# Performance work log

Measured on AMD Instinct MI355X. Metric: run time of the kernel, lower is better.

## Reference

```python
import jax, jax.numpy as jnp
import numpy as np

N = 4096
IN_DIM = 512
OUT_DIM = 64   # == d_head
HEADS = 8

def setup_inputs() -> dict:
    key = jax.random.key(0)
    ks = jax.random.split(key, 6)
    hd = OUT_DIM * HEADS  # 512
    s = 1.0 / np.sqrt(IN_DIM)
    x  = jax.random.normal(ks[0], (N, IN_DIM), dtype=jnp.float32)
    Wq = jax.random.uniform(ks[1], (hd, IN_DIM), minval=-s, maxval=s, dtype=jnp.float32)
    Wk = jax.random.uniform(ks[2], (hd, IN_DIM), minval=-s, maxval=s, dtype=jnp.float32)
    Wv = jax.random.uniform(ks[3], (hd, IN_DIM), minval=-s, maxval=s, dtype=jnp.float32)
    so = 1.0 / np.sqrt(hd)
    Wo = jax.random.uniform(ks[4], (OUT_DIM, hd), minval=-so, maxval=so, dtype=jnp.float32)
    bo = jax.random.uniform(ks[5], (OUT_DIM,), minval=-so, maxval=so, dtype=jnp.float32)
    return {"x": x, "Wq": Wq, "Wk": Wk, "Wv": Wv, "Wo": Wo, "bo": bo}

def reference(x, Wq, Wk, Wv, Wo, bo):
    n = x.shape[0]
    d_head = OUT_DIM
    Q = (x @ Wq.T).reshape(n, HEADS, d_head)
    K = (x @ Wk.T).reshape(n, HEADS, d_head)
    V = (x @ Wv.T).reshape(n, HEADS, d_head)
    # full softmax attention over all N nodes, per head
    attn = jnp.einsum('nhd,mhd->nhm', Q, K) / jnp.sqrt(jnp.float32(d_head))
    attn = jax.nn.softmax(attn, axis=-1)  # dropout p=0.0 -> identity
    out = jnp.einsum('nhm,mhd->nhd', attn, V)
    return out.reshape(n, HEADS * d_head) @ Wo.T + bo
```

## Files before the change

### kernel.cpp

```cpp
#include <hip/hip_runtime.h>

typedef unsigned short u16;
typedef unsigned int u32;
typedef __attribute__((ext_vector_type(8))) short bf16x8;
typedef __attribute__((ext_vector_type(4))) float f32x4;
typedef __attribute__((ext_vector_type(16))) float f32x16;
typedef __attribute__((ext_vector_type(4))) unsigned short u16x4;
typedef __attribute__((ext_vector_type(4))) unsigned int u32x4;

#define NSPLIT 8

__device__ __forceinline__ u16 f2b(float f) {
  u32 u = __builtin_bit_cast(u32, f);
  u32 r = (u + 0x7FFFu + ((u >> 16) & 1u)) >> 16;
  return (u16)r;
}

__device__ __forceinline__ f32x4 mfma16(bf16x8 a, bf16x8 b, f32x4 c) {
  return __builtin_amdgcn_mfma_f32_16x16x32_bf16(a, b, c, 0, 0, 0);
}
__device__ __forceinline__ f32x16 mfma32(bf16x8 a, bf16x8 b, f32x16 c) {
  return __builtin_amdgcn_mfma_f32_32x32x16_bf16(a, b, c, 0, 0, 0);
}
__device__ __forceinline__ u32 cvtpk(float lo, float hi) {
  u32 r;
  asm("v_cvt_pk_bf16_f32 %0, %1, %2" : "=v"(r) : "v"(lo), "v"(hi));
  return r;
}
__device__ __forceinline__ void pl32swap(u32& a, u32& b) {
  asm("v_permlane32_swap_b32 %0, %1" : "+v"(a), "+v"(b));
}

__global__ __launch_bounds__(256) void prep_kernel(
    const float* __restrict__ x, const float* __restrict__ wq,
    const float* __restrict__ wk, const float* __restrict__ Wo,
    const float* __restrict__ Wv,
    u16* __restrict__ xf, u16* __restrict__ wqf, u16* __restrict__ wkf,
    u16* __restrict__ wvof) {
  if (blockIdx.x < 1280) {
    int i = blockIdx.x * 256 + threadIdx.x;
    const float* src; u16* dst; int off; float scale = 1.0f;
    if (i < 262144)      { src = x;  dst = xf;  off = i; }
    else if (i < 294912) { src = wq; dst = wqf; off = i - 262144; scale = 0.18033688011112042f; }
    else                 { src = wk; dst = wkf; off = i - 294912; }
    int row = off >> 6;
    int c = (off & 63) * 8;
    int blk = row >> 4, lr = row & 15, kk = c >> 5, lg = (c >> 3) & 3;
    size_t fidx = ((((size_t)blk * 16 + kk) * 4 + lg) * 16 + lr) * 8;
    const float4* s4 = (const float4*)src;
    float4 a = s4[off * 2], b = s4[off * 2 + 1];
    u16x4 r0, r1;
    r0.x = f2b(a.x * scale); r0.y = f2b(a.y * scale);
    r0.z = f2b(a.z * scale); r0.w = f2b(a.w * scale);
    r1.x = f2b(b.x * scale); r1.y = f2b(b.y * scale);
    r1.z = f2b(b.z * scale); r1.w = f2b(b.w * scale);
    *(u16x4*)(dst + fidx) = r0;
    *(u16x4*)(dst + fidx + 4) = r1;
  } else {
    int t = (blockIdx.x - 1280) * 256 + threadIdx.x;
    int h = t >> 15, i = (t >> 9) & 63, j = t & 511;
    const float* worow = Wo + (size_t)i * 512 + h * 64;
    const float* wvcol = Wv + (size_t)(h * 64) * 512 + j;
    float s = 0.0f;
#pragma unroll 8
    for (int d = 0; d < 64; ++d) s += worow[d] * wvcol[(size_t)d * 512];
    int row = h * 64 + i;
    int cb = row >> 4, lr = row & 15, kk = j >> 5, lg = (j >> 3) & 3, jj = j & 7;
    wvof[((((size_t)cb * 16 + kk) * 4 + lg) * 16 + lr) * 8 + jj] = f2b(s);
  }
}

__global__ __launch_bounds__(256) void qkv_kernel(
    const u16* __restrict__ xf, const u16* __restrict__ wqf,
    const u16* __restrict__ wkf, const u16* __restrict__ wvof,
    u16* __restrict__ Qf, u16* __restrict__ Kf, u16* __restrict__ Vf) {
  int wave = threadIdx.x >> 6, lane = threadIdx.x & 63;
  int lr = lane & 15, lg = lane >> 4;
  int mode = blockIdx.y >> 2, cg = blockIdx.y & 3;
  const u16* W = (mode == 0) ? wqf : (mode == 1) ? wkf : wvof;
  f32x4 acc[2][8] = {};
  const u16* aB0 = xf + (size_t)(blockIdx.x * 8 + wave * 2) * 8192 + lg * 128 + lr * 8;
  const u16* bB0 = W + (size_t)(cg * 8) * 8192 + lg * 128 + lr * 8;
#pragma unroll 2
  for (int kk = 0; kk < 16; ++kk) {
    bf16x8 aF0 = *(const bf16x8*)(aB0 + kk * 512);
    bf16x8 aF1 = *(const bf16x8*)(aB0 + 8192 + kk * 512);
#pragma unroll
    for (int ni = 0; ni < 8; ++ni) {
      bf16x8 bF = *(const bf16x8*)(bB0 + (size_t)ni * 8192 + kk * 512);
      acc[0][ni] = mfma16(aF0, bF, acc[0][ni]);
      acc[1][ni] = mfma16(aF1, bF, acc[1][ni]);
    }
  }
  u16* dstBase = (mode == 0) ? Qf : (mode == 1) ? Kf : Vf;
#pragma unroll
  for (int rbi = 0; rbi < 2; ++rbi)
#pragma unroll
    for (int ni = 0; ni < 8; ++ni)
#pragma unroll
      for (int r = 0; r < 4; ++r) {
        int row = blockIdx.x * 128 + wave * 32 + rbi * 16 + lg * 4 + r;
        int colm = cg * 128 + ni * 16 + lr;
        int h = colm >> 6, d = colm & 63;
        u16 v = f2b(acc[rbi][ni][r]);
        u16* dst = dstBase + (size_t)h * 262144;
        if (mode < 2) {
          int kb = row >> 5, l31 = row & 31, s = (d >> 4) & 3, hi2 = (d >> 3) & 1, j = d & 7;
          dst[(((size_t)(kb * 4 + s) * 2 + hi2) * 32 + l31) * 8 + j] = v;
        } else {
          int kt = row >> 6, ks = (row >> 4) & 3, hi2 = (row >> 3) & 1, j = row & 7;
          dst[(((size_t)(kt * 4 + ks) * 2 + hi2) * 64 + d) * 8 + j] = v;
        }
      }
}

__global__ __launch_bounds__(256) void attn_kernel(
    const u16* __restrict__ Qf, const u16* __restrict__ Kf,
    const u16* __restrict__ Vf, float* __restrict__ Pacc,
    float* __restrict__ Pl) {
  int bid = blockIdx.x;
  int h = bid & 7, idx = bid >> 3;
  int c = idx & 7, qb = idx >> 3;
  int warp = threadIdx.x >> 6, lane = threadIdx.x & 63;
  int l31 = lane & 31, hi = lane >> 5;
  int q = qb * 128 + warp * 32 + l31;
  const u16* Qh = Qf + (size_t)h * 262144;
  const u16* Kh = Kf + (size_t)h * 262144;
  const u16* Vh = Vf + (size_t)h * 262144;

  int qb32 = qb * 4 + warp;
  bf16x8 qf[4];
#pragma unroll
  for (int s = 0; s < 4; ++s)
    qf[s] = *(const bf16x8*)(Qh + ((size_t)(qb32 * 4 + s) * 2 + hi) * 256 + l31 * 8);

  bf16x8 ka[4], kb[4];
  {
    int kb0 = (c * 512) >> 5;
#pragma unroll
    for (int s = 0; s < 4; ++s) {
      ka[s] = *(const bf16x8*)(Kh + ((size_t)(kb0 * 4 + s) * 2 + hi) * 256 + l31 * 8);
      kb[s] = *(const bf16x8*)(Kh + ((size_t)((kb0 + 1) * 4 + s) * 2 + hi) * 256 + l31 * 8);
    }
  }

  f32x16 o0 = {}, o1 = {};
  float l = 0.0f;

  for (int mt = 0; mt < 8; ++mt) {
    int kbase = c * 512 + mt * 64;
    int kt = kbase >> 6;
    f32x16 s0 = {}, s1 = {};
#pragma unroll
    for (int s = 0; s < 4; ++s) {
      s0 = mfma32(ka[s], qf[s], s0);
      s1 = mfma32(kb[s], qf[s], s1);
    }
    bf16x8 na[4], nb[4];
    if (mt < 7) {
      int nb0 = (kbase + 64) >> 5;
#pragma unroll
      for (int s = 0; s < 4; ++s) {
        na[s] = *(const bf16x8*)(Kh + ((size_t)(nb0 * 4 + s) * 2 + hi) * 256 + l31 * 8);
        nb[s] = *(const bf16x8*)(Kh + ((size_t)((nb0 + 1) * 4 + s) * 2 + hi) * 256 + l31 * 8);
      }
    }
    bf16x8 vf0[4], vf1[4];
#pragma unroll
    for (int ks = 0; ks < 4; ++ks) {
      const u16* vB = Vh + ((size_t)(kt * 4 + ks) * 2 + hi) * 512;
      vf0[ks] = *(const bf16x8*)(vB + l31 * 8);
      vf1[ks] = *(const bf16x8*)(vB + 256 + l31 * 8);
    }
#pragma unroll
    for (int r = 0; r < 16; ++r) s0[r] = __builtin_amdgcn_exp2f(s0[r]);
#pragma unroll
    for (int r = 0; r < 16; ++r) s1[r] = __builtin_amdgcn_exp2f(s1[r]);
    float u8[8];
#pragma unroll
    for (int i = 0; i < 8; ++i)
      u8[i] = (s0[i] + s0[i + 8]) + (s1[i] + s1[i + 8]);
    l += ((u8[0] + u8[1]) + (u8[2] + u8[3])) + ((u8[4] + u8[5]) + (u8[6] + u8[7]));
    u32 w[16];
#pragma unroll
    for (int i = 0; i < 8; ++i) {
      w[i]     = cvtpk(s0[2 * i], s0[2 * i + 1]);
      w[8 + i] = cvtpk(s1[2 * i], s1[2 * i + 1]);
    }
#pragma unroll
    for (int ks = 0; ks < 4; ++ks) {
      u32 a0 = w[4 * ks], b0 = w[4 * ks + 2];
      u32 a1 = w[4 * ks + 1], b1 = w[4 * ks + 3];
      pl32swap(a0, b0);
      pl32swap(a1, b1);
      u32x4 pw = {a0, a1, b0, b1};
      bf16x8 pb = __builtin_bit_cast(bf16x8, pw);
      o0 = mfma32(vf0[ks], pb, o0);
      o1 = mfma32(vf1[ks], pb, o1);
    }
#pragma unroll
    for (int s = 0; s < 4; ++s) { ka[s] = na[s]; kb[s] = nb[s]; }
  }
  l += __shfl_xor(l, 32);
  float* base = Pacc + ((size_t)(c * 8 + h) * 4096 + q) * 64;
#pragma unroll
  for (int g = 0; g < 4; ++g) {
    f32x4 v0 = {o0[4*g], o0[4*g+1], o0[4*g+2], o0[4*g+3]};
    f32x4 v1 = {o1[4*g], o1[4*g+1], o1[4*g+2], o1[4*g+3]};
    *(f32x4*)(base + 8 * g + 4 * hi) = v0;
    *(f32x4*)(base + 32 + 8 * g + 4 * hi) = v1;
  }
  if (!hi) Pl[(size_t)(c * 8 + h) * 4096 + q] = l;
}

__global__ __launch_bounds__(256) void combine_kernel(
    const float* __restrict__ Pacc, const float* __restrict__ Pl,
    const float* __restrict__ bo, float* __restrict__ out) {
  int t = blockIdx.x * 256 + threadIdx.x;
  int n = t >> 4, dp = (t & 15) * 4;
  f32x4 acc = {0, 0, 0, 0};
#pragma unroll
  for (int h = 0; h < 8; ++h) {
    float lt = 0.0f;
#pragma unroll
    for (int cc = 0; cc < NSPLIT; ++cc)
      lt += Pl[(size_t)(cc * 8 + h) * 4096 + n];
    float inv = 1.0f / lt;
    f32x4 oh = {0, 0, 0, 0};
#pragma unroll
    for (int cc = 0; cc < NSPLIT; ++cc) {
      f32x4 a = *(const f32x4*)(Pacc + (size_t)(cc * 8 + h) * 262144 + (size_t)n * 64 + dp);
      oh.x += a.x; oh.y += a.y; oh.z += a.z; oh.w += a.w;
    }
    acc.x += oh.x * inv; acc.y += oh.y * inv;
    acc.z += oh.z * inv; acc.w += oh.w * inv;
  }
  f32x4 b4 = *(const f32x4*)(bo + dp);
  acc.x += b4.x; acc.y += b4.y; acc.z += b4.z; acc.w += b4.w;
  *(f32x4*)(out + (size_t)n * 64 + dp) = acc;
}

extern "C" void kernel_launch(void* const* d_in, const int* in_sizes, int n_in,
                              void* d_out, int out_size, void* d_ws, size_t ws_size,
                              hipStream_t stream) {
  const float* x  = (const float*)d_in[0];
  const float* Wq = (const float*)d_in[1];
  const float* Wk = (const float*)d_in[2];
  const float* Wv = (const float*)d_in[3];
  const float* Wo = (const float*)d_in[4];
  const float* bo = (const float*)d_in[5];
  float* out = (float*)d_out;

  u16* xf   = (u16*)d_ws;
  u16* wqf  = xf + 2097152;
  u16* wkf  = wqf + 262144;
  u16* wvof = wkf + 262144;
  u16* Qf   = wvof + 262144;
  u16* Kf   = Qf + 2097152;
  u16* Vf   = Kf + 2097152;
  float* Pacc = (float*)(Vf + 2097152);
  float* Pl   = Pacc + (size_t)NSPLIT * 8 * 4096 * 64;
  (void)in_sizes; (void)n_in; (void)out_size; (void)ws_size;

  prep_kernel<<<2304, 256, 0, stream>>>(x, Wq, Wk, Wo, Wv, xf, wqf, wkf, wvof);
  qkv_kernel<<<dim3(32, 12), 256, 0, stream>>>(xf, wqf, wkf, wvof, Qf, Kf, Vf);
  attn_kernel<<<2048, 256, 0, stream>>>(Qf, Kf, Vf, Pacc, Pl);
  combine_kernel<<<256, 256, 0, stream>>>(Pacc, Pl, bo, out);
}
```

Before: 146.1 us.

## Stage QKV epilogue through LDS for vector stores; halve attention key splits

The QKV kernel now writes its accumulators into a swizzled shared-memory tile and then emits 16-byte vectorized global stores in the fragment layouts, replacing scattered 2-byte stores. The attention kernel drops from 8 to 4 key splits, so each block handles 1024 keys and the grid halves. The key loop is also restructured into a double-buffered helper that avoids register copies. Fewer splits shrink the partial-output traffic the combine kernel must read, at the cost of less parallelism and longer per-block serial work.

Result: faster. 137.4 us (-5.9%).

```diff
diff --git a/kernel.cpp b/kernel.cpp
--- a/kernel.cpp
+++ b/kernel.cpp
@@ -8,7 +8,7 @@
 typedef __attribute__((ext_vector_type(4))) unsigned short u16x4;
 typedef __attribute__((ext_vector_type(4))) unsigned int u32x4;
 
-#define NSPLIT 8
+#define NSPLIT 4
 
 __device__ __forceinline__ u16 f2b(float f) {
   u32 u = __builtin_bit_cast(u32, f);
@@ -70,10 +70,15 @@
   }
 }
 
+__device__ __forceinline__ int swz(int row, int colu16) {
+  return row * 256 + (((colu16) * 2) ^ ((row & 15) << 4));
+}
+
 __global__ __launch_bounds__(256) void qkv_kernel(
     const u16* __restrict__ xf, const u16* __restrict__ wqf,
     const u16* __restrict__ wkf, const u16* __restrict__ wvof,
     u16* __restrict__ Qf, u16* __restrict__ Kf, u16* __restrict__ Vf) {
+  __shared__ __align__(16) char tile[128 * 256];
   int wave = threadIdx.x >> 6, lane = threadIdx.x & 63;
   int lr = lane & 15, lg = lane >> 4;
   int mode = blockIdx.y >> 2, cg = blockIdx.y & 3;
@@ -92,26 +97,112 @@
       acc[1][ni] = mfma16(aF1, bF, acc[1][ni]);
     }
   }
+#pragma unroll
+  for (int rbi = 0; rbi < 2; ++rbi)
+#pragma unroll
+    for (int ni = 0; ni < 8; ++ni)
+#pragma unroll
+      for (int r = 0; r < 4; ++r) {
+        int row = wave * 32 + rbi * 16 + lg * 4 + r;
+        int col = ni * 16 + lr;
+        *(u16*)(tile + swz(row, col)) = f2b(acc[rbi][ni][r]);
+      }
+  __syncthreads();
   u16* dstBase = (mode == 0) ? Qf : (mode == 1) ? Kf : Vf;
-#pragma unroll
-  for (int rbi = 0; rbi < 2; ++rbi)
-#pragma unroll
-    for (int ni = 0; ni < 8; ++ni)
-#pragma unroll
-      for (int r = 0; r < 4; ++r) {
-        int row = blockIdx.x * 128 + wave * 32 + rbi * 16 + lg * 4 + r;
-        int colm = cg * 128 + ni * 16 + lr;
-        int h = colm >> 6, d = colm & 63;
-        u16 v = f2b(acc[rbi][ni][r]);
-        u16* dst = dstBase + (size_t)h * 262144;
-        if (mode < 2) {
-          int kb = row >> 5, l31 = row & 31, s = (d >> 4) & 3, hi2 = (d >> 3) & 1, j = d & 7;
-          dst[(((size_t)(kb * 4 + s) * 2 + hi2) * 32 + l31) * 8 + j] = v;
-        } else {
-          int kt = row >> 6, ks = (row >> 4) & 3, hi2 = (row >> 3) & 1, j = row & 7;
-          dst[(((size_t)(kt * 4 + ks) * 2 + hi2) * 64 + d) * 8 + j] = v;
-        }
+  if (mode < 2) {
+#pragma unroll
+    for (int it = 0; it < 8; ++it) {
+      int gid = wave * 8 + it;
+      int hh = gid >> 4, kbl = (gid >> 2) & 3, s = gid & 3;
+      int hi2 = lane >> 5, l31 = lane & 31;
+      int lrow = kbl * 32 + l31;
+      int col = hh * 64 + s * 16 + hi2 * 8;
+      u32x4 v = *(const u32x4*)(tile + swz(lrow, col));
+      int h = cg * 2 + hh, kb = blockIdx.x * 4 + kbl;
+      u16* dst = dstBase + (size_t)h * 262144 +
+                 (((size_t)(kb * 4 + s) * 2 + hi2) * 32 + l31) * 8;
+      *(u32x4*)dst = v;
+    }
+  } else {
+#pragma unroll
+    for (int it = 0; it < 8; ++it) {
+      int gid = wave * 8 + it;
+      int hh = gid >> 4, ktl = (gid >> 3) & 1, ks = (gid >> 1) & 3, hi2v = gid & 1;
+      int d = lane;
+      int r0 = ktl * 64 + ks * 16 + hi2v * 8;
+      int col = hh * 64 + d;
+      u32 wd[4];
+#pragma unroll
+      for (int jp = 0; jp < 4; ++jp) {
+        u32 lo = *(const u16*)(tile + swz(r0 + 2 * jp, col));
+        u32 hi = *(const u16*)(tile + swz(r0 + 2 * jp + 1, col));
+        wd[jp] = lo | (hi << 16);
       }
+      int h = cg * 2 + hh, kt = blockIdx.x * 2 + ktl;
+      u16* dst = dstBase + (size_t)h * 262144 +
+                 (((size_t)(kt * 4 + ks) * 2 + hi2v) * 64 + d) * 8;
+      u32x4 v = {wd[0], wd[1], wd[2], wd[3]};
+      *(u32x4*)dst = v;
+    }
+  }
+}
+
+struct KBuf { bf16x8 a[4], b[4]; };
+
+template <bool DOPREF>
+__device__ __forceinline__ void attn_step(
+    const u16* __restrict__ Kh, const u16* __restrict__ Vh,
+    const bf16x8 (&qf)[4], KBuf& cur, KBuf& nxt,
+    int kbase, int hi, int l31,
+    f32x16& o0, f32x16& o1, float& l) {
+  int kt = kbase >> 6;
+  f32x16 s0 = {}, s1 = {};
+#pragma unroll
+  for (int s = 0; s < 4; ++s) {
+    s0 = mfma32(cur.a[s], qf[s], s0);
+    s1 = mfma32(cur.b[s], qf[s], s1);
+  }
+  if (DOPREF) {
+    int nb0 = (kbase + 64) >> 5;
+#pragma unroll
+    for (int s = 0; s < 4; ++s) {
+      nxt.a[s] = *(const bf16x8*)(Kh + ((size_t)(nb0 * 4 + s) * 2 + hi) * 256 + l31 * 8);
+      nxt.b[s] = *(const bf16x8*)(Kh + ((size_t)((nb0 + 1) * 4 + s) * 2 + hi) * 256 + l31 * 8);
+    }
+  }
+  bf16x8 vf0[4], vf1[4];
+#pragma unroll
+  for (int ks = 0; ks < 4; ++ks) {
+    const u16* vB = Vh + ((size_t)(kt * 4 + ks) * 2 + hi) * 512;
+    vf0[ks] = *(const bf16x8*)(vB + l31 * 8);
+    vf1[ks] = *(const bf16x8*)(vB + 256 + l31 * 8);
+  }
+#pragma unroll
+  for (int r = 0; r < 16; ++r) s0[r] = __builtin_amdgcn_exp2f(s0[r]);
+#pragma unroll
+  for (int r = 0; r < 16; ++r) s1[r] = __builtin_amdgcn_exp2f(s1[r]);
+  float u8[8];
+#pragma unroll
+  for (int i = 0; i < 8; ++i)
+    u8[i] = (s0[i] + s0[i + 8]) + (s1[i] + s1[i + 8]);
+  l += ((u8[0] + u8[1]) + (u8[2] + u8[3])) + ((u8[4] + u8[5]) + (u8[6] + u8[7]));
+  u32 w[16];
+#pragma unroll
+  for (int i = 0; i < 8; ++i) {
+    w[i]     = cvtpk(s0[2 * i], s0[2 * i + 1]);
+    w[8 + i] = cvtpk(s1[2 * i], s1[2 * i + 1]);
+  }
+#pragma unroll
+  for (int ks = 0; ks < 4; ++ks) {
+    u32 a0 = w[4 * ks], b0 = w[4 * ks + 2];
+    u32 a1 = w[4 * ks + 1], b1 = w[4 * ks + 3];
+    pl32swap(a0, b0);
+    pl32swap(a1, b1);
+    u32x4 pw = {a0, a1, b0, b1};
+    bf16x8 pb = __builtin_bit_cast(bf16x8, pw);
+    o0 = mfma32(vf0[ks], pb, o0);
+    o1 = mfma32(vf1[ks], pb, o1);
+  }
 }
 
 __global__ __launch_bounds__(256) void attn_kernel(
@@ -120,7 +211,7 @@
     float* __restrict__ Pl) {
   int bid = blockIdx.x;
   int h = bid & 7, idx = bid >> 3;
-  int c = idx & 7, qb = idx >> 3;
+  int c = idx & 3, qb = idx >> 2;
   int warp = threadIdx.x >> 6, lane = threadIdx.x & 63;
   int l31 = lane & 31, hi = lane >> 5;
   int q = qb * 128 + warp * 32 + l31;
@@ -134,73 +225,28 @@
   for (int s = 0; s < 4; ++s)
     qf[s] = *(const bf16x8*)(Qh + ((size_t)(qb32 * 4 + s) * 2 + hi) * 256 + l31 * 8);
 
-  bf16x8 ka[4], kb[4];
+  KBuf buf0, buf1;
   {
-    int kb0 = (c * 512) >> 5;
+    int kb0 = (c * 1024) >> 5;
 #pragma unroll
     for (int s = 0; s < 4; ++s) {
-      ka[s] = *(const bf16x8*)(Kh + ((size_t)(kb0 * 4 + s) * 2 + hi) * 256 + l31 * 8);
-      kb[s] = *(const bf16x8*)(Kh + ((size_t)((kb0 + 1) * 4 + s) * 2 + hi) * 256 + l31 * 8);
+      buf0.a[s] = *(const bf16x8*)(Kh + ((size_t)(kb0 * 4 + s) * 2 + hi) * 256 + l31 * 8);
+      buf0.b[s] = *(const bf16x8*)(Kh + ((size_t)((kb0 + 1) * 4 + s) * 2 + hi) * 256 + l31 * 8);
     }
   }
 
   f32x16 o0 = {}, o1 = {};
   float l = 0.0f;
 
-  for (int mt = 0; mt < 8; ++mt) {
-    int kbase = c * 512 + mt * 64;
-    int kt = kbase >> 6;
-    f32x16 s0 = {}, s1 = {};
-#pragma unroll
-    for (int s = 0; s < 4; ++s) {
-      s0 = mfma32(ka[s], qf[s], s0);
-      s1 = mfma32(kb[s], qf[s], s1);
-    }
-    bf16x8 na[4], nb[4];
-    if (mt < 7) {
-      int nb0 = (kbase + 64) >> 5;
-#pragma unroll
-      for (int s = 0; s < 4; ++s) {
-        na[s] = *(const bf16x8*)(Kh + ((size_t)(nb0 * 4 + s) * 2 + hi) * 256 + l31 * 8);
-        nb[s] = *(const bf16x8*)(Kh + ((size_t)((nb0 + 1) * 4 + s) * 2 + hi) * 256 + l31 * 8);
-      }
-    }
-    bf16x8 vf0[4], vf1[4];
-#pragma unroll
-    for (int ks = 0; ks < 4; ++ks) {
-      const u16* vB = Vh + ((size_t)(kt * 4 + ks) * 2 + hi) * 512;
-      vf0[ks] = *(const bf16x8*)(vB + l31 * 8);
-      vf1[ks] = *(const bf16x8*)(vB + 256 + l31 * 8);
-    }
-#pragma unroll
-    for (int r = 0; r < 16; ++r) s0[r] = __builtin_amdgcn_exp2f(s0[r]);
-#pragma unroll
-    for (int r = 0; r < 16; ++r) s1[r] = __builtin_amdgcn_exp2f(s1[r]);
-    float u8[8];
-#pragma unroll
-    for (int i = 0; i < 8; ++i)
-      u8[i] = (s0[i] + s0[i + 8]) + (s1[i] + s1[i + 8]);
-    l += ((u8[0] + u8[1]) + (u8[2] + u8[3])) + ((u8[4] + u8[5]) + (u8[6] + u8[7]));
-    u32 w[16];
-#pragma unroll
-    for (int i = 0; i < 8; ++i) {
-      w[i]     = cvtpk(s0[2 * i], s0[2 * i + 1]);
-      w[8 + i] = cvtpk(s1[2 * i], s1[2 * i + 1]);
-    }
-#pragma unroll
-    for (int ks = 0; ks < 4; ++ks) {
-      u32 a0 = w[4 * ks], b0 = w[4 * ks + 2];
-      u32 a1 = w[4 * ks + 1], b1 = w[4 * ks + 3];
-      pl32swap(a0, b0);
-      pl32swap(a1, b1);
-      u32x4 pw = {a0, a1, b0, b1};
-      bf16x8 pb = __builtin_bit_cast(bf16x8, pw);
-      o0 = mfma32(vf0[ks], pb, o0);
-      o1 = mfma32(vf1[ks], pb, o1);
-    }
-#pragma unroll
-    for (int s = 0; s < 4; ++s) { ka[s] = na[s]; kb[s] = nb[s]; }
-  }
+  int cb = c * 1024;
+  for (int mt2 = 0; mt2 < 7; ++mt2) {
+    int kbase = cb + mt2 * 128;
+    attn_step<true>(Kh, Vh, qf, buf0, buf1, kbase, hi, l31, o0, o1, l);
+    attn_step<true>(Kh, Vh, qf, buf1, buf0, kbase + 64, hi, l31, o0, o1, l);
+  }
+  attn_step<true >(Kh, Vh, qf, buf0, buf1, cb + 896, hi, l31, o0, o1, l);
+  attn_step<false>(Kh, Vh, qf, buf1, buf0, cb + 960, hi, l31, o0, o1, l);
+
   l += __shfl_xor(l, 32);
   float* base = Pacc + ((size_t)(c * 8 + h) * 4096 + q) * 64;
 #pragma unroll
@@ -264,6 +310,6 @@
 
   prep_kernel<<<2304, 256, 0, stream>>>(x, Wq, Wk, Wo, Wv, xf, wqf, wkf, wvof);
   qkv_kernel<<<dim3(32, 12), 256, 0, stream>>>(xf, wqf, wkf, wvof, Qf, Kf, Vf);
-  attn_kernel<<<2048, 256, 0, stream>>>(Qf, Kf, Vf, Pacc, Pl);
+  attn_kernel<<<1024, 256, 0, stream>>>(Qf, Kf, Vf, Pacc, Pl);
   combine_kernel<<<256, 256, 0, stream>>>(Pacc, Pl, bo, out);
 }
```
